# Kernel optimization log

Measured on AMD Instinct MI355X. Metric: run time of the kernel, lower is better.

## Reference

```python
import jax, jax.numpy as jnp
import numpy as np

N_NODES = 100000
N_EDGES = 3200000
D_FEAT = 512
HIDDEN = 16
N_CLASSES = 16


def setup_inputs() -> dict:
    key = jax.random.key(0)
    ks = jax.random.split(key, 6)
    x = jax.random.normal(ks[0], (N_NODES, D_FEAT), dtype=jnp.float32)
    edge_index = jax.random.randint(ks[1], (2, N_EDGES), 0, N_NODES, dtype=jnp.int64)
    edge_weight = jax.random.uniform(ks[2], (N_EDGES,), dtype=jnp.float32)
    W1 = jax.random.normal(ks[3], (D_FEAT, HIDDEN), dtype=jnp.float32) * (1.0 / np.sqrt(D_FEAT))
    b1 = jnp.zeros((HIDDEN,), dtype=jnp.float32)
    W2 = jax.random.normal(ks[4], (HIDDEN, N_CLASSES), dtype=jnp.float32) * (1.0 / np.sqrt(HIDDEN))
    b2 = jnp.zeros((N_CLASSES,), dtype=jnp.float32)
    return {"x": x, "edge_index": edge_index, "edge_weight": edge_weight,
            "W1": W1, "b1": b1, "W2": W2, "b2": b2}


def _gcn_conv(h, src, dst, edge_weight, W, b, num_nodes):
    # linear transform then edge-weighted scatter-add: out[dst] += w_e * (h W)[src]
    h = h @ W                                   # [N, out]
    msg = edge_weight[:, None] * h[src]         # [E, out] gather + scale
    out = jax.ops.segment_sum(msg, dst, num_segments=num_nodes)  # scatter-add
    return out + b


def reference(x, edge_index, edge_weight, W1, b1, W2, b2):
    src, dst = edge_index[0], edge_index[1]
    n = x.shape[0]
    h = jax.nn.relu(_gcn_conv(x, src, dst, edge_weight, W1, b1, n))
    # dropout is identity in eval mode
    h = _gcn_conv(h, src, dst, edge_weight, W2, b2, n)
    return jax.nn.log_softmax(h, axis=1)
```

## Files before the change

kernel.cpp:

```cpp
#include <hip/hip_runtime.h>
#include <math.h>

#define NN 100000
#define DF 512
#define HID 16
#define NBUCK 392
#define EPB 4096
#define BCAP 7800

__device__ int g_idx64;

__global__ void detect_idx_kernel(const long long* __restrict__ idx) {
    int lane = threadIdx.x;
    int ok = 1;
    for (int i = lane; i < 128; i += 64) {
        long long v = idx[i];
        if (v < 0 || v >= NN) ok = 0;
    }
    unsigned long long m = __ballot(ok);
    if (lane == 0) g_idx64 = (m == ~0ULL);
}

__global__ __launch_bounds__(256) void gemm1_kernel(
    const float* __restrict__ x, const float* __restrict__ W1,
    float* __restrict__ h1, int nN)
{
    __shared__ float part[2][16 * 64];
    int w    = threadIdx.x >> 6;
    int lane = threadIdx.x & 63;
    int pair = w >> 1;
    int half = w & 1;
    int node = blockIdx.x * 128 + pair * 64 + lane;
    bool alive = node < nN;

    float acc[16];
#pragma unroll
    for (int c = 0; c < 16; ++c) acc[c] = 0.f;

    if (alive) {
        const float4* xr = (const float4*)(x + (size_t)node * DF) + half * (DF / 8);
        const float* wb = W1 + half * (DF / 2) * HID;
#pragma unroll 4
        for (int kq = 0; kq < DF / 8; ++kq) {
            float4 xv = xr[kq];
            const float* wrow = wb + kq * 4 * HID;
            float xs[4] = {xv.x, xv.y, xv.z, xv.w};
#pragma unroll
            for (int j = 0; j < 4; ++j) {
                float s = xs[j];
#pragma unroll
                for (int c = 0; c < 16; ++c)
                    acc[c] = fmaf(s, wrow[j * 16 + c], acc[c]);
            }
        }
    }
    if (half == 1) {
#pragma unroll
        for (int c = 0; c < 16; ++c) part[pair][c * 64 + lane] = acc[c];
    }
    __syncthreads();
    if (half == 0 && alive) {
#pragma unroll
        for (int c = 0; c < 16; ++c) acc[c] += part[pair][c * 64 + lane];
        float4* o = (float4*)(h1 + (size_t)node * HID);
#pragma unroll
        for (int g = 0; g < 4; ++g)
            o[g] = make_float4(acc[g * 4 + 0], acc[g * 4 + 1],
                               acc[g * 4 + 2], acc[g * 4 + 3]);
    }
}

__global__ __launch_bounds__(256) void bucket_hist_kernel(
    const void* __restrict__ eidx, int* __restrict__ bcnt, int nE)
{
    __shared__ int h[NBUCK];
    for (int i = threadIdx.x; i < NBUCK; i += 256) h[i] = 0;
    __syncthreads();
    const int i64 = g_idx64;
    int stride = gridDim.x * 256;
    int tid = blockIdx.x * 256 + threadIdx.x;
    if ((nE & 1) == 0) {
        int nE2 = nE >> 1;
        if (i64) {
            const int4* dp = (const int4*)((const long long*)eidx + nE);
            for (int i = tid; i < nE2; i += stride) {
                int4 d = dp[i];
                if (d.y == 0 && (unsigned)d.x < (unsigned)NN) atomicAdd(&h[d.x >> 8], 1);
                if (d.w == 0 && (unsigned)d.z < (unsigned)NN) atomicAdd(&h[d.z >> 8], 1);
            }
        } else {
            const int2* dp = (const int2*)((const int*)eidx + nE);
            for (int i = tid; i < nE2; i += stride) {
                int2 d = dp[i];
                if ((unsigned)d.x < (unsigned)NN) atomicAdd(&h[d.x >> 8], 1);
                if ((unsigned)d.y < (unsigned)NN) atomicAdd(&h[d.y >> 8], 1);
            }
        }
    } else {
        for (int e = tid; e < nE; e += stride) {
            int d;
            if (i64) d = (int)((const long long*)eidx)[nE + e];
            else     d = ((const int*)eidx)[nE + e];
            if ((unsigned)d < (unsigned)NN) atomicAdd(&h[d >> 8], 1);
        }
    }
    __syncthreads();
    for (int i = threadIdx.x; i < NBUCK; i += 256)
        if (h[i]) atomicAdd(&bcnt[i], h[i]);
}

__global__ __launch_bounds__(512) void bucket_scan_kernel(
    const int* __restrict__ bcnt, int* __restrict__ bbase,
    int* __restrict__ cursor, int* __restrict__ rowStart)
{
    __shared__ int s[512];
    int t = threadIdx.x;
    int v = (t < NBUCK) ? bcnt[t] : 0;
    s[t] = v;
    __syncthreads();
    for (int off = 1; off < 512; off <<= 1) {
        int u = (t >= off) ? s[t - off] : 0;
        __syncthreads();
        s[t] += u;
        __syncthreads();
    }
    int excl = s[t] - v;
    if (t < NBUCK) { bbase[t] = excl; cursor[t] = excl; }
    if (t == NBUCK) bbase[t] = excl;
    if (t == NBUCK) rowStart[NN] = excl;
}

__global__ __launch_bounds__(256) void bucketA_kernel(
    const void* __restrict__ eidx, const float* __restrict__ ew,
    int* __restrict__ cursor, int2* __restrict__ packed, int nE)
{
    __shared__ int cnt[NBUCK];
    __shared__ int base[NBUCK];
    int t = threadIdx.x;
    for (int i = t; i < NBUCK; i += 256) cnt[i] = 0;
    __syncthreads();

    const int e0 = blockIdx.x * EPB;
    const int i64 = g_idx64;
    int lo[16]; float wv[16]; int bk[16];
#pragma unroll
    for (int i = 0; i < 16; ++i) {
        int e = e0 + t + i * 256;
        bk[i] = -1;
        if (e < nE) {
            int s, d;
            if (i64) {
                const long long* p = (const long long*)eidx;
                s = (int)p[e]; d = (int)p[nE + e];
            } else {
                const int* p = (const int*)eidx;
                s = p[e]; d = p[nE + e];
            }
            if ((unsigned)d < (unsigned)NN) {
                float w = ew[e];
                if ((unsigned)s >= (unsigned)NN) { s = 0; w = 0.f; }
                bk[i] = d >> 8;
                lo[i] = s | ((d & 255) << 20);
                wv[i] = w;
                atomicAdd(&cnt[bk[i]], 1);
            }
        }
    }
    __syncthreads();
    for (int i = t; i < NBUCK; i += 256)
        base[i] = (cnt[i] > 0) ? atomicAdd(&cursor[i], cnt[i]) : 0;
    __syncthreads();
    for (int i = t; i < NBUCK; i += 256) cnt[i] = 0;
    __syncthreads();
#pragma unroll
    for (int i = 0; i < 16; ++i) {
        if (bk[i] >= 0) {
            int r = atomicAdd(&cnt[bk[i]], 1);
            packed[base[bk[i]] + r] = make_int2(lo[i], __float_as_int(wv[i]));
        }
    }
}

__global__ __launch_bounds__(256) void bucketB_kernel(
    const int2* __restrict__ packed, const int* __restrict__ bbase,
    int* __restrict__ rowStart, int2* __restrict__ se, int nN)
{
    __shared__ int hcnt[256];
    __shared__ int wtot[4];
    __shared__ int2 stage[BCAP];
    int b = blockIdx.x;
    int t = threadIdx.x;
    int beg = bbase[b], end = bbase[b + 1];
    int cnt = end - beg;

    hcnt[t] = 0;
    __syncthreads();
    for (int i = t; i < cnt; i += 256) {
        int2 e = packed[beg + i];
        if (i < BCAP) stage[i] = e;
        atomicAdd(&hcnt[(e.x >> 20) & 255], 1);
    }
    __syncthreads();

    int v = hcnt[t];
    int incl = v;
#pragma unroll
    for (int off = 1; off < 64; off <<= 1) {
        int u = __shfl_up(incl, off, 64);
        if ((t & 63) >= off) incl += u;
    }
    if ((t & 63) == 63) wtot[t >> 6] = incl;
    __syncthreads();
    int woff = 0;
#pragma unroll
    for (int w = 0; w < 4; ++w) if (w < (t >> 6)) woff += wtot[w];
    int excl = incl - v + woff;

    int node = b * 256 + t;
    if (node < nN) rowStart[node] = beg + excl;
    __syncthreads();
    hcnt[t] = beg + excl;
    __syncthreads();

    for (int i = t; i < cnt; i += 256) {
        int2 e = (i < BCAP) ? stage[i] : packed[beg + i];
        int dl = (e.x >> 20) & 255;
        int pos = atomicAdd(&hcnt[dl], 1);
        se[pos] = make_int2(e.x & 0xFFFFF, e.y);
    }
}

template <int EPI>
__global__ __launch_bounds__(256) void gather_fused_kernel(
    const int* __restrict__ rowStart, const int2* __restrict__ se,
    const float* __restrict__ h, const float* __restrict__ bias,
    const float* __restrict__ Wn, float* __restrict__ outp, int nN)
{
    __shared__ float sW[256];
    __shared__ float sb[16];
    if (EPI == 0) sW[threadIdx.x] = Wn[threadIdx.x];
    if (threadIdx.x < 16) sb[threadIdx.x] = bias[threadIdx.x];
    __syncthreads();

    int t = blockIdx.x * 256 + threadIdx.x;
    int n = t >> 2;
    if (n >= nN) return;
    int c4 = t & 3;
    int beg = rowStart[n], end = rowStart[n + 1];
    const float4* h4 = (const float4*)h;

    float ax = 0.f, ay = 0.f, az = 0.f, aw = 0.f;
    int p = beg;
    for (; p + 4 <= end; p += 4) {
        int2 e0 = se[p], e1 = se[p + 1], e2 = se[p + 2], e3 = se[p + 3];
        float4 v0 = h4[(size_t)(unsigned)e0.x * 4 + c4];
        float4 v1 = h4[(size_t)(unsigned)e1.x * 4 + c4];
        float4 v2 = h4[(size_t)(unsigned)e2.x * 4 + c4];
        float4 v3 = h4[(size_t)(unsigned)e3.x * 4 + c4];
        float w0 = __int_as_float(e0.y), w1 = __int_as_float(e1.y);
        float w2 = __int_as_float(e2.y), w3 = __int_as_float(e3.y);
        ax = fmaf(w0, v0.x, ax); ay = fmaf(w0, v0.y, ay);
        az = fmaf(w0, v0.z, az); aw = fmaf(w0, v0.w, aw);
        ax = fmaf(w1, v1.x, ax); ay = fmaf(w1, v1.y, ay);
        az = fmaf(w1, v1.z, az); aw = fmaf(w1, v1.w, aw);
        ax = fmaf(w2, v2.x, ax); ay = fmaf(w2, v2.y, ay);
        az = fmaf(w2, v2.z, az); aw = fmaf(w2, v2.w, aw);
        ax = fmaf(w3, v3.x, ax); ay = fmaf(w3, v3.y, ay);
        az = fmaf(w3, v3.z, az); aw = fmaf(w3, v3.w, aw);
    }
    for (; p < end; ++p) {
        int2 e = se[p];
        float4 v = h4[(size_t)(unsigned)e.x * 4 + c4];
        float w = __int_as_float(e.y);
        ax = fmaf(w, v.x, ax); ay = fmaf(w, v.y, ay);
        az = fmaf(w, v.z, az); aw = fmaf(w, v.w, aw);
    }

    int lane = threadIdx.x & 63;
    int lb = lane & ~3;

    if (EPI == 0) {
        float v0 = fmaxf(ax + sb[c4 * 4 + 0], 0.f);
        float v1 = fmaxf(ay + sb[c4 * 4 + 1], 0.f);
        float v2 = fmaxf(az + sb[c4 * 4 + 2], 0.f);
        float v3 = fmaxf(aw + sb[c4 * 4 + 3], 0.f);
        float vk[16];
#pragma unroll
        for (int j = 0; j < 4; ++j) {
            vk[4 * j + 0] = __shfl(v0, lb + j, 64);
            vk[4 * j + 1] = __shfl(v1, lb + j, 64);
            vk[4 * j + 2] = __shfl(v2, lb + j, 64);
            vk[4 * j + 3] = __shfl(v3, lb + j, 64);
        }
        float o0 = 0.f, o1 = 0.f, o2 = 0.f, o3 = 0.f;
#pragma unroll
        for (int k = 0; k < 16; ++k) {
            float s = vk[k];
            o0 = fmaf(s, sW[k * 16 + c4 * 4 + 0], o0);
            o1 = fmaf(s, sW[k * 16 + c4 * 4 + 1], o1);
            o2 = fmaf(s, sW[k * 16 + c4 * 4 + 2], o2);
            o3 = fmaf(s, sW[k * 16 + c4 * 4 + 3], o3);
        }
        ((float4*)outp)[(size_t)n * 4 + c4] = make_float4(o0, o1, o2, o3);
    } else {
        float v0 = ax + sb[c4 * 4 + 0];
        float v1 = ay + sb[c4 * 4 + 1];
        float v2 = az + sb[c4 * 4 + 2];
        float v3 = aw + sb[c4 * 4 + 3];
        float m = fmaxf(fmaxf(v0, v1), fmaxf(v2, v3));
        m = fmaxf(m, __shfl_xor(m, 1, 64));
        m = fmaxf(m, __shfl_xor(m, 2, 64));
        float s = expf(v0 - m) + expf(v1 - m) + expf(v2 - m) + expf(v3 - m);
        s += __shfl_xor(s, 1, 64);
        s += __shfl_xor(s, 2, 64);
        float l = m + logf(s);
        ((float4*)outp)[(size_t)n * 4 + c4] =
            make_float4(v0 - l, v1 - l, v2 - l, v3 - l);
    }
}

extern "C" void kernel_launch(void* const* d_in, const int* in_sizes, int n_in,
                              void* d_out, int out_size, void* d_ws, size_t ws_size,
                              hipStream_t stream)
{
    const float* x  = (const float*)d_in[0];
    const void*  ei = d_in[1];
    const float* ew = (const float*)d_in[2];
    const float* W1 = (const float*)d_in[3];
    const float* b1 = (const float*)d_in[4];
    const float* W2 = (const float*)d_in[5];
    const float* b2 = (const float*)d_in[6];
    float* out = (float*)d_out;

    const int N = NN;
    const int E = in_sizes[2];

    const size_t featB = (size_t)N * HID * sizeof(float);
    const size_t rowB  = (((size_t)(N + 1) * 4) + 255) & ~255ULL;
    const size_t bkB   = (((size_t)(NBUCK + 1) * 4) + 255) & ~255ULL;
    const size_t seB   = ((size_t)E * 8 + 255) & ~255ULL;

    char* w = (char*)d_ws;
    float* buf0 = (float*)w;      w += (featB + 255) & ~255ULL;
    float* buf1 = (float*)w;      w += (featB + 255) & ~255ULL;
    int*   rowStart = (int*)w;    w += rowB;
    int*   bcnt = (int*)w;        w += bkB;
    int*   bbase = (int*)w;       w += bkB;
    int*   cursor = (int*)w;      w += bkB;
    int2*  se = (int2*)w;         w += seB;
    int2*  packed = (int2*)w;     w += seB;

    detect_idx_kernel<<<1, 64, 0, stream>>>((const long long*)ei);
    gemm1_kernel<<<(N + 127) / 128, 256, 0, stream>>>(x, W1, buf0, N);

    const int nblocks4 = (N * 4 + 255) / 256;

    hipMemsetAsync(bcnt, 0, (size_t)NBUCK * 4, stream);
    bucket_hist_kernel<<<256, 256, 0, stream>>>(ei, bcnt, E);
    bucket_scan_kernel<<<1, 512, 0, stream>>>(bcnt, bbase, cursor, rowStart);
    bucketA_kernel<<<(E + EPB - 1) / EPB, 256, 0, stream>>>(ei, ew, cursor, packed, E);
    bucketB_kernel<<<NBUCK, 256, 0, stream>>>(packed, bbase, rowStart, se, N);

    gather_fused_kernel<0><<<nblocks4, 256, 0, stream>>>(rowStart, se, buf0, b1, W2, buf1, N);
    gather_fused_kernel<1><<<nblocks4, 256, 0, stream>>>(rowStart, se, buf1, b2, W2, out, N);
}
```

Measured before the change: 603.8 us.

## Stage x tiles through LDS with coalesced loads and register prefetch in GEMM1

The first linear layer previously had each thread stream its own node's row of x, so every wavefront load touched 64 different rows. It now loads 128-node by 64-feature chunks cooperatively, with 16 threads per row for coalesced float4 reads. Each chunk goes into padded shared memory, and the next chunk is prefetched into registers while the current one is consumed. This adds LDS traffic and two barriers per chunk in exchange for better global-memory coalescing on the 200MB x read.

```diff
diff --git a/kernel.cpp b/kernel.cpp
--- a/kernel.cpp
+++ b/kernel.cpp
@@ -8,6 +8,11 @@
 #define EPB 4096
 #define BCAP 7800
 
+#define TN 128
+#define KC 64
+#define NCH (DF / KC)
+#define LROW 65
+
 __device__ int g_idx64;
 
 __global__ void detect_idx_kernel(const long long* __restrict__ idx) {
@@ -25,48 +30,75 @@
     const float* __restrict__ x, const float* __restrict__ W1,
     float* __restrict__ h1, int nN)
 {
-    __shared__ float part[2][16 * 64];
-    int w    = threadIdx.x >> 6;
-    int lane = threadIdx.x & 63;
-    int pair = w >> 1;
-    int half = w & 1;
-    int node = blockIdx.x * 128 + pair * 64 + lane;
-    bool alive = node < nN;
+    __shared__ float sx[TN * LROW];
+    __shared__ float part[TN * 17];
+    const int t = threadIdx.x;
+    const int tr = t >> 4;
+    const int tq = t & 15;
+    const int node0 = blockIdx.x * TN;
+    const int node = t & (TN - 1);
+    const int half = t >> 7;
+
+    const float4* x4 = (const float4*)x;
+    int rowg[8];
+#pragma unroll
+    for (int i = 0; i < 8; ++i) {
+        int r = node0 + i * 16 + tr;
+        rowg[i] = (r < nN) ? r : (nN - 1);
+    }
+
+    float4 pf[8];
+#pragma unroll
+    for (int i = 0; i < 8; ++i)
+        pf[i] = x4[(size_t)rowg[i] * (DF / 4) + tq];
 
     float acc[16];
 #pragma unroll
     for (int c = 0; c < 16; ++c) acc[c] = 0.f;
 
-    if (alive) {
-        const float4* xr = (const float4*)(x + (size_t)node * DF) + half * (DF / 8);
-        const float* wb = W1 + half * (DF / 2) * HID;
-#pragma unroll 4
-        for (int kq = 0; kq < DF / 8; ++kq) {
-            float4 xv = xr[kq];
-            const float* wrow = wb + kq * 4 * HID;
-            float xs[4] = {xv.x, xv.y, xv.z, xv.w};
-#pragma unroll
-            for (int j = 0; j < 4; ++j) {
-                float s = xs[j];
-#pragma unroll
-                for (int c = 0; c < 16; ++c)
-                    acc[c] = fmaf(s, wrow[j * 16 + c], acc[c]);
-            }
-        }
-    }
+    for (int kc = 0; kc < NCH; ++kc) {
+#pragma unroll
+        for (int i = 0; i < 8; ++i) {
+            int a = (i * 16 + tr) * LROW + tq * 4;
+            sx[a + 0] = pf[i].x; sx[a + 1] = pf[i].y;
+            sx[a + 2] = pf[i].z; sx[a + 3] = pf[i].w;
+        }
+        __syncthreads();
+        if (kc + 1 < NCH) {
+            int qb = (kc + 1) * 16 + tq;
+#pragma unroll
+            for (int i = 0; i < 8; ++i)
+                pf[i] = x4[(size_t)rowg[i] * (DF / 4) + qb];
+        }
+        const float* wb = W1 + (kc * KC + half * 32) * HID;
+        const float* xr = sx + node * LROW + half * 32;
+#pragma unroll 8
+        for (int kk = 0; kk < 32; ++kk) {
+            float s = xr[kk];
+            const float* wr = wb + kk * HID;
+#pragma unroll
+            for (int c = 0; c < 16; ++c)
+                acc[c] = fmaf(s, wr[c], acc[c]);
+        }
+        __syncthreads();
+    }
+
     if (half == 1) {
 #pragma unroll
-        for (int c = 0; c < 16; ++c) part[pair][c * 64 + lane] = acc[c];
-    }
-    __syncthreads();
-    if (half == 0 && alive) {
-#pragma unroll
-        for (int c = 0; c < 16; ++c) acc[c] += part[pair][c * 64 + lane];
-        float4* o = (float4*)(h1 + (size_t)node * HID);
-#pragma unroll
-        for (int g = 0; g < 4; ++g)
-            o[g] = make_float4(acc[g * 4 + 0], acc[g * 4 + 1],
-                               acc[g * 4 + 2], acc[g * 4 + 3]);
+        for (int c = 0; c < 16; ++c) part[node * 17 + c] = acc[c];
+    }
+    __syncthreads();
+    if (half == 0) {
+        int gn = node0 + node;
+        if (gn < nN) {
+#pragma unroll
+            for (int c = 0; c < 16; ++c) acc[c] += part[node * 17 + c];
+            float4* o = (float4*)(h1 + (size_t)gn * HID);
+#pragma unroll
+            for (int g = 0; g < 4; ++g)
+                o[g] = make_float4(acc[g * 4 + 0], acc[g * 4 + 1],
+                                   acc[g * 4 + 2], acc[g * 4 + 3]);
+        }
     }
 }
 
@@ -351,7 +383,7 @@
     int2*  packed = (int2*)w;     w += seB;
 
     detect_idx_kernel<<<1, 64, 0, stream>>>((const long long*)ei);
-    gemm1_kernel<<<(N + 127) / 128, 256, 0, stream>>>(x, W1, buf0, N);
+    gemm1_kernel<<<(N + TN - 1) / TN, 256, 0, stream>>>(x, W1, buf0, N);
 
     const int nblocks4 = (N * 4 + 255) / 256;
 
```

After: 613.4 us. About the same (+1.6%).
